# Performance work log

Hardware: AMD Instinct MI355X
Metric: run time of the kernel (lower is better)

The kernel has to match this reference:

```python
import math
import jax, jax.numpy as jnp
import numpy as np

H = 8
DIM = 256
HD = DIM // H
SCALE = math.sqrt(HD)
EPS = 1e-16


def _segment_softmax(scores, dst, num_nodes):
    # scores: [E, H], dst: [E] -> softmax over edges sharing the same dst
    m = jax.ops.segment_max(scores, dst, num_segments=num_nodes)  # [N, H]
    m = jnp.where(jnp.isfinite(m), m, 0.0)  # empty segments -> -inf -> 0
    e = jnp.exp(scores - m[dst])
    s = jax.ops.segment_sum(e, dst, num_segments=num_nodes)  # [N, H]
    return e / (s[dst] + EPS)


def _graph_attention(x, edges, wq, bq, wk, bk, wv, bv, wo, bo):
    # x: [N, DIM]; edges: [2, E] (src, dst). Dropout is identity (eval mode).
    N = x.shape[0]
    Q = (x @ wq + bq).reshape(N, H, HD)
    K = (x @ wk + bk).reshape(N, H, HD)
    V = (x @ wv + bv).reshape(N, H, HD)
    src, dst = edges[0], edges[1]
    scores = jnp.einsum('ehd,ehd->eh', Q[dst], K[src]) / SCALE  # [E, H]
    attn = _segment_softmax(scores, dst, N)  # [E, H]
    msgs = V[src] * attn[:, :, None]  # [E, H, HD]
    out = jax.ops.segment_sum(msgs, dst, num_segments=N).reshape(N, DIM)
    return out @ wo + bo


def _linear_params(key, fan_in, fan_out):
    k1, k2 = jax.random.split(key)
    bound = 1.0 / math.sqrt(fan_in)
    w = jax.random.uniform(k1, (fan_in, fan_out), minval=-bound, maxval=bound, dtype=jnp.float32)
    b = jax.random.uniform(k2, (fan_out,), minval=-bound, maxval=bound, dtype=jnp.float32)
    return w, b


def setup_inputs() -> dict:
    key = jax.random.key(0)
    ks = jax.random.split(key, 12)
    n_slot, n_dom = 20000, 1000
    e_slot, e_dom = 320000, 16000
    inp = {
        'slot_x': jax.random.normal(ks[0], (n_slot, DIM), dtype=jnp.float32),
        'domain_x': jax.random.normal(ks[1], (n_dom, DIM), dtype=jnp.float32),
        'slot_edges': jax.random.randint(ks[2], (2, e_slot), 0, n_slot, dtype=jnp.int32),
        'domain_edges': jax.random.randint(ks[3], (2, e_dom), 0, n_dom, dtype=jnp.int32),
    }
    names = ['wq', 'wk', 'wv', 'wo']
    for i, nm in enumerate(names):
        w, b = _linear_params(ks[4 + i], DIM, DIM)
        inp[f'slot_{nm}'] = w
        inp[f'slot_{nm}_b'] = b
    for i, nm in enumerate(names):
        w, b = _linear_params(ks[8 + i], DIM, DIM)
        inp[f'dom_{nm}'] = w
        inp[f'dom_{nm}_b'] = b
    return inp


def reference(slot_x, domain_x, slot_edges, domain_edges,
              slot_wq, slot_wq_b, slot_wk, slot_wk_b, slot_wv, slot_wv_b, slot_wo, slot_wo_b,
              dom_wq, dom_wq_b, dom_wk, dom_wk_b, dom_wv, dom_wv_b, dom_wo, dom_wo_b):
    # slot branch: self-attention on slot graph + identity residual
    slot_out = _graph_attention(slot_x, slot_edges,
                                slot_wq, slot_wq_b, slot_wk, slot_wk_b,
                                slot_wv, slot_wv_b, slot_wo, slot_wo_b) + slot_x
    # domain branch
    dom_out = _graph_attention(domain_x, domain_edges,
                               dom_wq, dom_wq_b, dom_wk, dom_wk_b,
                               dom_wv, dom_wv_b, dom_wo, dom_wo_b) + domain_x
    return slot_out, dom_out
```

## Files before the change

kernel.cpp:

```cpp
#include <hip/hip_runtime.h>
#include <hip/hip_bf16.h>

#define DIM 256
#define INV_SCALE 0.17677669529663687f
#define SM_EPS 1e-16f
#define BM 128
#define BN 64
#define BK 32

typedef unsigned short ushortT;
typedef unsigned int uintT;
typedef __attribute__((ext_vector_type(8))) __bf16 bf16x8;
typedef __attribute__((ext_vector_type(4))) float f32x4;

__device__ __forceinline__ float bf2f(ushortT u) {
    return __uint_as_float(((uintT)u) << 16);
}
__device__ __forceinline__ ushortT f2bf(float f) {
    uintT u = __float_as_uint(f);
    u += 0x7FFFu + ((u >> 16) & 1u);
    return (ushortT)(u >> 16);
}

struct WPack { const void* w[8]; const void* b[8]; };

__device__ __forceinline__ bool sniff_m16(const ushortT* __restrict__ x) {
    int lane = threadIdx.x & 63;
    ushortT u = x[lane * 2];
    int e = (u >> 7) & 0xFF;
    bool sane = ((u & 0x7FFFu) == 0) || (e >= 0x66 && e <= 0x90);
    unsigned long long m = __ballot(sane);
    return __popcll(m) >= 32;
}

__global__ __launch_bounds__(256) void megaA(
        const void* __restrict__ xs, const void* __restrict__ xd,
        const ushortT* __restrict__ sniff_src,
        ushortT* __restrict__ xb_s, ushortT* __restrict__ xb_d,
        WPack pk, ushortT* __restrict__ wT, float* __restrict__ biasF,
        int* __restrict__ cnt_s, int* __restrict__ cnt_d,
        uintT* __restrict__ st_s, uintT* __restrict__ st_d,
        int* __restrict__ done, int* __restrict__ flagWs,
        int n4s, int n4d, int Ns_, int Nd_, int nbN_, int nbD_,
        int nA0, int nA1, int nA2)
{
    const bool m16 = sniff_m16(sniff_src);
    const int bid = blockIdx.x;
    const int t = threadIdx.x;

    if (bid < nA0 + nA1) {
        const bool d = bid >= nA0;
        const int li = d ? bid - nA0 : bid;
        const int n4 = d ? n4d : n4s;
        const int i = li * 256 + t;
        if (i >= n4) return;
        const void* x = d ? xd : xs;
        ushortT* xb = d ? xb_d : xb_s;
        if (m16) {
            ((ushort4*)xb)[i] = ((const ushort4*)x)[i];
        } else {
            float4 v = ((const float4*)x)[i];
            ushort4 o2;
            o2.x = f2bf(v.x); o2.y = f2bf(v.y); o2.z = f2bf(v.z); o2.w = f2bf(v.w);
            ((ushort4*)xb)[i] = o2;
        }
    } else if (bid < nA0 + nA1 + nA2) {
        const int r = bid - (nA0 + nA1);
        const int which = r / 257;
        const int j = r % 257;
        if (j == 256) {
            const void* b = pk.b[which];
            float v = m16 ? bf2f(((const ushortT*)b)[t]) : ((const float*)b)[t];
            biasF[which * 256 + t] = v;
        } else {
            const void* w = pk.w[which];
            float v = m16 ? bf2f(((const ushortT*)w)[t * 256 + j])
                          : ((const float*)w)[t * 256 + j];
            wT[(size_t)which * 65536 + j * 256 + t] = f2bf(v);
        }
    } else {
        const int li = bid - (nA0 + nA1 + nA2);
        const int idx = li * 256 + t;
        if (idx < Ns_) { cnt_s[idx] = 0; return; }
        int k = idx - Ns_;
        if (k < Nd_) { cnt_d[k] = 0; return; }
        k -= Nd_;
        if (k < nbN_) { st_s[k] = 0; return; }
        k -= nbN_;
        if (k < nbD_) { st_d[k] = 0; return; }
        k -= nbD_;
        if (k == 0) *done = 0;
        else if (k == 1) *flagWs = m16 ? 1 : 0;
    }
}

__device__ __forceinline__ void gemm_core(const ushortT* __restrict__ A,
                                          const ushortT* __restrict__ BT,
                                          int row0, int col0, int M,
                                          f32x4 (&acc)[2][4]) {
    __shared__ ushortT As[BM * BK];
    __shared__ ushortT Bs[BN * BK];
    const int tid  = threadIdx.x;
    const int wid  = tid >> 6;
    const int lane = tid & 63;
    const int r_i = tid >> 2;
    const int kq8 = (tid & 3) << 3;
    const int m   = lane & 15;
    const int q   = lane >> 4;

    const size_t rA0 = (size_t)min(row0 + r_i, M - 1) * DIM;
    const size_t rA1 = (size_t)min(row0 + 64 + r_i, M - 1) * DIM;
    const size_t rB  = (size_t)(col0 + r_i) * DIM;

    for (int k0 = 0; k0 < DIM; k0 += BK) {
        uint4 a0v = *(const uint4*)(A + rA0 + k0 + kq8);
        uint4 a1v = *(const uint4*)(A + rA1 + k0 + kq8);
        uint4 bv  = *(const uint4*)(BT + rB + k0 + kq8);
        __syncthreads();
        *(uint4*)&As[r_i * BK + kq8]        = a0v;
        *(uint4*)&As[(64 + r_i) * BK + kq8] = a1v;
        *(uint4*)&Bs[r_i * BK + kq8]        = bv;
        __syncthreads();

        bf16x8 af0 = *(const bf16x8*)&As[(wid * 32 + m) * BK + q * 8];
        bf16x8 af1 = *(const bf16x8*)&As[(wid * 32 + 16 + m) * BK + q * 8];
        #pragma unroll
        for (int j = 0; j < 4; ++j) {
            bf16x8 bf = *(const bf16x8*)&Bs[(j * 16 + m) * BK + q * 8];
            acc[0][j] = __builtin_amdgcn_mfma_f32_16x16x32_bf16(af0, bf, acc[0][j], 0, 0, 0);
            acc[1][j] = __builtin_amdgcn_mfma_f32_16x16x32_bf16(af1, bf, acc[1][j], 0, 0, 0);
        }
    }
}

__global__ __launch_bounds__(256) void megaB(
        const ushortT* __restrict__ xb_s, const ushortT* __restrict__ xb_d,
        const ushortT* __restrict__ wT, const float* __restrict__ biasF,
        ushortT* __restrict__ qkv_s, ushortT* __restrict__ qkv_d,
        size_t zss, size_t zsd, int Ms, int Md, int nbs_, int nbq_,
        const int* __restrict__ dst_s, const int* __restrict__ dst_d,
        int* __restrict__ cnt_s, int* __restrict__ cnt_d, int Es_, int Ed_)
{
    const int bid = blockIdx.x;
    const int nq = nbq_ * 12;
    if (bid >= nq) {
        const int idx = (bid - nq) * 256 + threadIdx.x;
        if (idx < Es_) atomicAdd(&cnt_s[dst_s[idx]], 1);
        else { int e = idx - Es_; if (e < Ed_) atomicAdd(&cnt_d[dst_d[e]], 1); }
        return;
    }
    const int z  = bid / (nbq_ * 4);
    const int r  = bid % (nbq_ * 4);
    const int by = r / nbq_;
    const int bx0 = r % nbq_;
    const bool dom = bx0 >= nbs_;
    const int bx = dom ? bx0 - nbs_ : bx0;
    const ushortT* A = dom ? xb_d : xb_s;
    const int M = dom ? Md : Ms;
    const int widx = z + (dom ? 4 : 0);
    const ushortT* BT = wT + (size_t)widx * 65536;
    const float* bias = biasF + widx * 256;
    ushortT* C = (dom ? qkv_d : qkv_s) + (size_t)z * (dom ? zsd : zss);

    const int row0 = bx * BM;
    const int col0 = by * BN;
    const int wid = threadIdx.x >> 6, lane = threadIdx.x & 63;
    const int m = lane & 15, q = lane >> 4;

    f32x4 acc[2][4];
    #pragma unroll
    for (int i = 0; i < 2; ++i)
        #pragma unroll
        for (int j = 0; j < 4; ++j) acc[i][j] = (f32x4){0.f, 0.f, 0.f, 0.f};

    gemm_core(A, BT, row0, col0, M, acc);

    #pragma unroll
    for (int i = 0; i < 2; ++i)
        #pragma unroll
        for (int j = 0; j < 4; ++j) {
            const int col = col0 + j * 16 + m;
            const float bval = bias[col];
            #pragma unroll
            for (int rr = 0; rr < 4; ++rr) {
                const int row = row0 + wid * 32 + i * 16 + q * 4 + rr;
                if (row < M)
                    C[(size_t)row * DIM + col] = f2bf(acc[i][j][rr] + bval);
            }
        }
}

__device__ __forceinline__ uintT spack(uintT st, uintT v) { return (st << 30) | v; }

__global__ __launch_bounds__(256) void scan_scatter(
        const int* __restrict__ cnt_s, const int* __restrict__ cnt_d,
        uintT* __restrict__ st_s, uintT* __restrict__ st_d,
        int* __restrict__ rp_s, int* __restrict__ rp_d,
        int* __restrict__ cur_s, int* __restrict__ cur_d,
        int* __restrict__ done,
        const int* __restrict__ ss, const int* __restrict__ ds,
        const int* __restrict__ sd, const int* __restrict__ dd,
        int* __restrict__ col_s, int* __restrict__ col_d,
        int Ns_, int Nd_, int nbN_, int nbD_, int Es_, int Ed_)
{
    __shared__ int sh[256];
    __shared__ int exclS;
    const int b = blockIdx.x;
    const int t = threadIdx.x;
    const bool dom = b >= nbN_;
    const int lb = dom ? b - nbN_ : b;
    const int N = dom ? Nd_ : Ns_;
    const int* cnt = dom ? cnt_d : cnt_s;
    uintT* st = dom ? st_d : st_s;
    int* rp = dom ? rp_d : rp_s;
    int* cur = dom ? cur_d : cur_s;

    const int i = lb * 256 + t;
    const int v = (i < N) ? cnt[i] : 0;
    sh[t] = v;
    __syncthreads();
    for (int off = 1; off < 256; off <<= 1) {
        int u = (t >= off) ? sh[t - off] : 0;
        __syncthreads();
        sh[t] += u;
        __syncthreads();
    }

    if (t == 0) {
        const uintT agg = (uintT)sh[255];
        uintT excl = 0;
        if (lb == 0) {
            __hip_atomic_store(&st[0], spack(2u, agg), __ATOMIC_RELEASE,
                               __HIP_MEMORY_SCOPE_AGENT);
        } else {
            __hip_atomic_store(&st[lb], spack(1u, agg), __ATOMIC_RELEASE,
                               __HIP_MEMORY_SCOPE_AGENT);
            int j = lb - 1;
            while (j >= 0) {
                uintT s = __hip_atomic_load(&st[j], __ATOMIC_ACQUIRE,
                                            __HIP_MEMORY_SCOPE_AGENT);
                uintT tag = s >> 30;
                if (tag == 2u) { excl += s & 0x3FFFFFFFu; break; }
                if (tag == 1u) { excl += s & 0x3FFFFFFFu; --j; }
            }
            __hip_atomic_store(&st[lb], spack(2u, excl + agg), __ATOMIC_RELEASE,
                               __HIP_MEMORY_SCOPE_AGENT);
        }
        exclS = (int)excl;
    }
    __syncthreads();
    const int excl = exclS;
    if (i < N) {
        const int e = excl + ((t == 0) ? 0 : sh[t - 1]);
        rp[i] = e;
        cur[i] = e;
        if (i == N - 1) rp[N] = e + v;
    }

    __threadfence();
    __syncthreads();
    if (t == 0) {
        __hip_atomic_fetch_add(done, 1, __ATOMIC_ACQ_REL, __HIP_MEMORY_SCOPE_AGENT);
        const int nb = nbN_ + nbD_;
        while (__hip_atomic_load(done, __ATOMIC_ACQUIRE, __HIP_MEMORY_SCOPE_AGENT) < nb) {}
    }
    __syncthreads();

    const int total = Es_ + Ed_;
    const int stride = (nbN_ + nbD_) * 256;
    for (int idx = b * 256 + t; idx < total; idx += stride) {
        if (idx < Es_) {
            int pos = atomicAdd(&cur_s[ds[idx]], 1);
            col_s[pos] = ss[idx];
        } else {
            int e = idx - Es_;
            int pos = atomicAdd(&cur_d[dd[e]], 1);
            col_d[pos] = sd[e];
        }
    }
}

__global__ __launch_bounds__(256) void attn_kernel(
        const ushortT* __restrict__ Qs, const ushortT* __restrict__ Ks,
        const ushortT* __restrict__ Vs, const int* __restrict__ rps,
        const int* __restrict__ css, ushortT* __restrict__ aggs,
        const ushortT* __restrict__ Qd_, const ushortT* __restrict__ Kd_,
        const ushortT* __restrict__ Vd_, const int* __restrict__ rpd,
        const int* __restrict__ csd, ushortT* __restrict__ aggd,
        int Ns_, int Ntot)
{
    const int sub = threadIdx.x & 31;
    const int g = blockIdx.x * 8 + (threadIdx.x >> 5);
    if (g >= Ntot) return;
    const bool dom = g >= Ns_;
    const int d = dom ? g - Ns_ : g;
    const ushortT* Qb = dom ? Qd_ : Qs;
    const ushortT* Kb = dom ? Kd_ : Ks;
    const ushortT* Vb = dom ? Vd_ : Vs;
    const int* rowptr = dom ? rpd : rps;
    const int* colsrc = dom ? csd : css;
    ushortT* aggb = dom ? aggd : aggs;

    const int c8 = sub * 8;
    const size_t cbase = (size_t)d * DIM + c8;

    uint4 qv = *(const uint4*)(Qb + cbase);
    float qf[8];
    qf[0] = bf2f((ushortT)(qv.x & 0xFFFF)); qf[1] = bf2f((ushortT)(qv.x >> 16));
    qf[2] = bf2f((ushortT)(qv.y & 0xFFFF)); qf[3] = bf2f((ushortT)(qv.y >> 16));
    qf[4] = bf2f((ushortT)(qv.z & 0xFFFF)); qf[5] = bf2f((ushortT)(qv.z >> 16));
    qf[6] = bf2f((ushortT)(qv.w & 0xFFFF)); qf[7] = bf2f((ushortT)(qv.w >> 16));

    float acc[8] = {};
    float den = 0.f;

    auto PROC = [&](uint4 kv, uint4 vv) {
        float kf[8];
        kf[0] = bf2f((ushortT)(kv.x & 0xFFFF)); kf[1] = bf2f((ushortT)(kv.x >> 16));
        kf[2] = bf2f((ushortT)(kv.y & 0xFFFF)); kf[3] = bf2f((ushortT)(kv.y >> 16));
        kf[4] = bf2f((ushortT)(kv.z & 0xFFFF)); kf[5] = bf2f((ushortT)(kv.z >> 16));
        kf[6] = bf2f((ushortT)(kv.w & 0xFFFF)); kf[7] = bf2f((ushortT)(kv.w >> 16));
        float p = qf[0] * kf[0] + qf[1] * kf[1] + qf[2] * kf[2] + qf[3] * kf[3]
                + qf[4] * kf[4] + qf[5] * kf[5] + qf[6] * kf[6] + qf[7] * kf[7];
        p += __shfl_xor(p, 1, 4);
        p += __shfl_xor(p, 2, 4);
        const float w = __expf(fminf(p * INV_SCALE, 60.0f));
        den += w;
        acc[0] += w * bf2f((ushortT)(vv.x & 0xFFFF));
        acc[1] += w * bf2f((ushortT)(vv.x >> 16));
        acc[2] += w * bf2f((ushortT)(vv.y & 0xFFFF));
        acc[3] += w * bf2f((ushortT)(vv.y >> 16));
        acc[4] += w * bf2f((ushortT)(vv.z & 0xFFFF));
        acc[5] += w * bf2f((ushortT)(vv.z >> 16));
        acc[6] += w * bf2f((ushortT)(vv.w & 0xFFFF));
        acc[7] += w * bf2f((ushortT)(vv.w >> 16));
    };

    const int beg = rowptr[d], end = rowptr[d + 1];
    int i = beg;
    for (; i + 4 <= end; i += 4) {
        const int s0 = colsrc[i], s1 = colsrc[i + 1];
        const int s2 = colsrc[i + 2], s3 = colsrc[i + 3];
        const size_t b0 = (size_t)s0 * DIM + c8, b1 = (size_t)s1 * DIM + c8;
        const size_t b2 = (size_t)s2 * DIM + c8, b3 = (size_t)s3 * DIM + c8;
        uint4 k0v = *(const uint4*)(Kb + b0), v0v = *(const uint4*)(Vb + b0);
        uint4 k1v = *(const uint4*)(Kb + b1), v1v = *(const uint4*)(Vb + b1);
        uint4 k2v = *(const uint4*)(Kb + b2), v2v = *(const uint4*)(Vb + b2);
        uint4 k3v = *(const uint4*)(Kb + b3), v3v = *(const uint4*)(Vb + b3);
        PROC(k0v, v0v); PROC(k1v, v1v); PROC(k2v, v2v); PROC(k3v, v3v);
    }
    for (; i < end; ++i) {
        const size_t sb = (size_t)colsrc[i] * DIM + c8;
        PROC(*(const uint4*)(Kb + sb), *(const uint4*)(Vb + sb));
    }

    const float r = 1.0f / (den + SM_EPS);
    uint4 o;
    o.x = (uintT)f2bf(acc[0] * r) | ((uintT)f2bf(acc[1] * r) << 16);
    o.y = (uintT)f2bf(acc[2] * r) | ((uintT)f2bf(acc[3] * r) << 16);
    o.z = (uintT)f2bf(acc[4] * r) | ((uintT)f2bf(acc[5] * r) << 16);
    o.w = (uintT)f2bf(acc[6] * r) | ((uintT)f2bf(acc[7] * r) << 16);
    *(uint4*)(aggb + cbase) = o;
}

__global__ __launch_bounds__(256) void gemm_out(
        const ushortT* __restrict__ As_, const ushortT* __restrict__ Ad_,
        const ushortT* __restrict__ wT, const float* __restrict__ biasF,
        const void* __restrict__ xs, const void* __restrict__ xd,
        void* __restrict__ dout, int Ms, int Md, int nbs,
        const int* __restrict__ flag)
{
    const bool dom = (int)blockIdx.x >= nbs;
    const int bx = dom ? blockIdx.x - nbs : blockIdx.x;
    const ushortT* A = dom ? Ad_ : As_;
    const int M = dom ? Md : Ms;
    const int widx = 3 + (dom ? 4 : 0);
    const ushortT* BT = wT + (size_t)widx * 65536;
    const float* bias = biasF + widx * 256;
    const void* res = dom ? xd : xs;
    const size_t outOff = dom ? (size_t)Ms * DIM : 0;

    const int row0 = bx * BM;
    const int col0 = blockIdx.y * BN;
    const int wid = threadIdx.x >> 6, lane = threadIdx.x & 63;
    const int m = lane & 15, q = lane >> 4;

    f32x4 acc[2][4];
    #pragma unroll
    for (int i = 0; i < 2; ++i)
        #pragma unroll
        for (int j = 0; j < 4; ++j) acc[i][j] = (f32x4){0.f, 0.f, 0.f, 0.f};

    gemm_core(A, BT, row0, col0, M, acc);

    const bool m16 = (*flag != 0);
    #pragma unroll
    for (int i = 0; i < 2; ++i)
        #pragma unroll
        for (int j = 0; j < 4; ++j) {
            const int col = col0 + j * 16 + m;
            const float bval = bias[col];
            #pragma unroll
            for (int r = 0; r < 4; ++r) {
                const int row = row0 + wid * 32 + i * 16 + q * 4 + r;
                if (row < M) {
                    const size_t ridx = (size_t)row * DIM + col;
                    float v = acc[i][j][r] + bval;
                    v += m16 ? bf2f(((const ushortT*)res)[ridx])
                             : ((const float*)res)[ridx];
                    if (m16) ((ushortT*)dout)[outOff + ridx] = f2bf(v);
                    else     ((float*)dout)[outOff + ridx] = v;
                }
            }
        }
}

extern "C" void kernel_launch(void* const* d_in, const int* in_sizes, int n_in,
                              void* d_out, int out_size, void* d_ws, size_t ws_size,
                              hipStream_t stream)
{
    const void* slot_x = d_in[0];
    const void* dom_x  = d_in[1];
    const int* slot_edges = (const int*)d_in[2];
    const int* dom_edges  = (const int*)d_in[3];
    const int Ns = in_sizes[0] / DIM;
    const int Nd = in_sizes[1] / DIM;
    const int Es = in_sizes[2] / 2;
    const int Ed = in_sizes[3] / 2;

    WPack pk;
    for (int i = 0; i < 8; ++i) { pk.w[i] = d_in[4 + 2 * i]; pk.b[i] = d_in[5 + 2 * i]; }

    char* p = (char*)d_ws;
    size_t o = 0;
    auto take = [&](size_t b) { void* r = p + o; o = (o + b + 255) & ~(size_t)255; return r; };
    const size_t ndS = (size_t)Ns * DIM;
    const size_t ndD = (size_t)Nd * DIM;
    ushortT* xb_s  = (ushortT*)take(ndS * 2);
    ushortT* qkv_s = (ushortT*)take(3 * ndS * 2);
    ushortT* agg_s = (ushortT*)take(ndS * 2);
    ushortT* xb_d  = (ushortT*)take(ndD * 2);
    ushortT* qkv_d = (ushortT*)take(3 * ndD * 2);
    ushortT* agg_d = (ushortT*)take(ndD * 2);
    ushortT* wT    = (ushortT*)take(8 * 65536 * 2);
    float*   biasF = (float*)take(8 * 256 * 4);
    int* rp_s  = (int*)take((size_t)(Ns + 1) * 4);
    int* cur_s = (int*)take((size_t)Ns * 4);
    int* cnt_s = (int*)take((size_t)Ns * 4);
    int* col_s = (int*)take((size_t)Es * 4);
    int* rp_d  = (int*)take((size_t)(Nd + 1) * 4);
    int* cur_d = (int*)take((size_t)Nd * 4);
    int* cnt_d = (int*)take((size_t)Nd * 4);
    int* col_d = (int*)take((size_t)Ed * 4);
    uintT* st_s = (uintT*)take(512 * 4);
    uintT* st_d = (uintT*)take(256 * 4);
    int* done   = (int*)take(256);
    int* flagWs = (int*)take(256);

    const int* src_s = slot_edges;
    const int* dst_s = slot_edges + Es;
    const int* src_d = dom_edges;
    const int* dst_d = dom_edges + Ed;

    const int n4s = Ns * DIM / 4, n4d = Nd * DIM / 4;
    const int nbN = (Ns + 255) / 256;
    const int nbD = (Nd + 255) / 256;
    const int nbs = (Ns + BM - 1) / BM;
    const int nbd = (Nd + BM - 1) / BM;
    const int nbq = nbs + nbd;

    const int nA0 = (n4s + 255) / 256;
    const int nA1 = (n4d + 255) / 256;
    const int nA2 = 257 * 8;
    const int nZ  = (Ns + Nd + nbN + nbD + 2 + 255) / 256;
    hipLaunchKernelGGL(megaA, dim3(nA0 + nA1 + nA2 + nZ), dim3(256), 0, stream,
                       slot_x, dom_x, (const ushortT*)slot_x, xb_s, xb_d,
                       pk, wT, biasF, cnt_s, cnt_d, st_s, st_d, done, flagWs,
                       n4s, n4d, Ns, Nd, nbN, nbD, nA0, nA1, nA2);

    const int nCnt = (Es + Ed + 255) / 256;
    hipLaunchKernelGGL(megaB, dim3(nbq * 12 + nCnt), dim3(256), 0, stream,
                       xb_s, xb_d, wT, biasF, qkv_s, qkv_d, ndS, ndD,
                       Ns, Nd, nbs, nbq, dst_s, dst_d, cnt_s, cnt_d, Es, Ed);

    hipLaunchKernelGGL(scan_scatter, dim3(nbN + nbD), dim3(256), 0, stream,
                       cnt_s, cnt_d, st_s, st_d, rp_s, rp_d, cur_s, cur_d, done,
                       src_s, dst_s, src_d, dst_d, col_s, col_d,
                       Ns, Nd, nbN, nbD, Es, Ed);

    const int Ntot = Ns + Nd;
    hipLaunchKernelGGL(attn_kernel, dim3((Ntot + 7) / 8), dim3(256), 0, stream,
                       qkv_s, qkv_s + ndS, qkv_s + 2 * ndS, rp_s, col_s, agg_s,
                       qkv_d, qkv_d + ndD, qkv_d + 2 * ndD, rp_d, col_d, agg_d,
                       Ns, Ntot);

    hipLaunchKernelGGL(gemm_out, dim3(nbq, DIM / BN), dim3(256), 0, stream,
                       agg_s, agg_d, wT, biasF, slot_x, dom_x, d_out,
                       Ns, Nd, nbs, flagWs);
}
```

Baseline: 271.5 us.

## Split scan/scatter kernel at grid barrier and deepen attention gather unroll

The combined scan_scatter kernel used a spin-wait grid barrier on a global counter before scattering edges with only ~83 blocks. It is now split into scan_nodes and a separate scatter_edges kernel with one thread per edge, so the kernel boundary replaces the barrier and the scatter runs across many more blocks. The attention gather loop also gains an 8-edge unrolled stage that issues all K/V loads before processing them, to keep more memory requests in flight. The costs are one extra kernel launch and higher register pressure in the attention kernel.

```diff
diff --git a/kernel.cpp b/kernel.cpp
--- a/kernel.cpp
+++ b/kernel.cpp
@@ -192,16 +192,12 @@
 
 __device__ __forceinline__ uintT spack(uintT st, uintT v) { return (st << 30) | v; }
 
-__global__ __launch_bounds__(256) void scan_scatter(
+__global__ __launch_bounds__(256) void scan_nodes(
         const int* __restrict__ cnt_s, const int* __restrict__ cnt_d,
         uintT* __restrict__ st_s, uintT* __restrict__ st_d,
         int* __restrict__ rp_s, int* __restrict__ rp_d,
         int* __restrict__ cur_s, int* __restrict__ cur_d,
-        int* __restrict__ done,
-        const int* __restrict__ ss, const int* __restrict__ ds,
-        const int* __restrict__ sd, const int* __restrict__ dd,
-        int* __restrict__ col_s, int* __restrict__ col_d,
-        int Ns_, int Nd_, int nbN_, int nbD_, int Es_, int Ed_)
+        int Ns_, int Nd_, int nbN_)
 {
     __shared__ int sh[256];
     __shared__ int exclS;
@@ -256,24 +252,22 @@
         cur[i] = e;
         if (i == N - 1) rp[N] = e + v;
     }
-
-    __threadfence();
-    __syncthreads();
-    if (t == 0) {
-        __hip_atomic_fetch_add(done, 1, __ATOMIC_ACQ_REL, __HIP_MEMORY_SCOPE_AGENT);
-        const int nb = nbN_ + nbD_;
-        while (__hip_atomic_load(done, __ATOMIC_ACQUIRE, __HIP_MEMORY_SCOPE_AGENT) < nb) {}
-    }
-    __syncthreads();
-
-    const int total = Es_ + Ed_;
-    const int stride = (nbN_ + nbD_) * 256;
-    for (int idx = b * 256 + t; idx < total; idx += stride) {
-        if (idx < Es_) {
-            int pos = atomicAdd(&cur_s[ds[idx]], 1);
-            col_s[pos] = ss[idx];
-        } else {
-            int e = idx - Es_;
+}
+
+__global__ __launch_bounds__(256) void scatter_edges(
+        const int* __restrict__ ss, const int* __restrict__ ds,
+        const int* __restrict__ sd, const int* __restrict__ dd,
+        int* __restrict__ cur_s, int* __restrict__ cur_d,
+        int* __restrict__ col_s, int* __restrict__ col_d,
+        int Es_, int Ed_)
+{
+    const int idx = blockIdx.x * 256 + threadIdx.x;
+    if (idx < Es_) {
+        int pos = atomicAdd(&cur_s[ds[idx]], 1);
+        col_s[pos] = ss[idx];
+    } else {
+        int e = idx - Es_;
+        if (e < Ed_) {
             int pos = atomicAdd(&cur_d[dd[e]], 1);
             col_d[pos] = sd[e];
         }
@@ -338,16 +332,27 @@
 
     const int beg = rowptr[d], end = rowptr[d + 1];
     int i = beg;
+    for (; i + 8 <= end; i += 8) {
+        uint4 kv[8], vv[8];
+        #pragma unroll
+        for (int j = 0; j < 8; ++j) {
+            const size_t b = (size_t)colsrc[i + j] * DIM + c8;
+            kv[j] = *(const uint4*)(Kb + b);
+            vv[j] = *(const uint4*)(Vb + b);
+        }
+        #pragma unroll
+        for (int j = 0; j < 8; ++j) PROC(kv[j], vv[j]);
+    }
     for (; i + 4 <= end; i += 4) {
-        const int s0 = colsrc[i], s1 = colsrc[i + 1];
-        const int s2 = colsrc[i + 2], s3 = colsrc[i + 3];
-        const size_t b0 = (size_t)s0 * DIM + c8, b1 = (size_t)s1 * DIM + c8;
-        const size_t b2 = (size_t)s2 * DIM + c8, b3 = (size_t)s3 * DIM + c8;
-        uint4 k0v = *(const uint4*)(Kb + b0), v0v = *(const uint4*)(Vb + b0);
-        uint4 k1v = *(const uint4*)(Kb + b1), v1v = *(const uint4*)(Vb + b1);
-        uint4 k2v = *(const uint4*)(Kb + b2), v2v = *(const uint4*)(Vb + b2);
-        uint4 k3v = *(const uint4*)(Kb + b3), v3v = *(const uint4*)(Vb + b3);
-        PROC(k0v, v0v); PROC(k1v, v1v); PROC(k2v, v2v); PROC(k3v, v3v);
+        uint4 kv[4], vv[4];
+        #pragma unroll
+        for (int j = 0; j < 4; ++j) {
+            const size_t b = (size_t)colsrc[i + j] * DIM + c8;
+            kv[j] = *(const uint4*)(Kb + b);
+            vv[j] = *(const uint4*)(Vb + b);
+        }
+        #pragma unroll
+        for (int j = 0; j < 4; ++j) PROC(kv[j], vv[j]);
     }
     for (; i < end; ++i) {
         const size_t sb = (size_t)colsrc[i] * DIM + c8;
@@ -483,10 +488,12 @@
                        xb_s, xb_d, wT, biasF, qkv_s, qkv_d, ndS, ndD,
                        Ns, Nd, nbs, nbq, dst_s, dst_d, cnt_s, cnt_d, Es, Ed);
 
-    hipLaunchKernelGGL(scan_scatter, dim3(nbN + nbD), dim3(256), 0, stream,
-                       cnt_s, cnt_d, st_s, st_d, rp_s, rp_d, cur_s, cur_d, done,
-                       src_s, dst_s, src_d, dst_d, col_s, col_d,
-                       Ns, Nd, nbN, nbD, Es, Ed);
+    hipLaunchKernelGGL(scan_nodes, dim3(nbN + nbD), dim3(256), 0, stream,
+                       cnt_s, cnt_d, st_s, st_d, rp_s, rp_d, cur_s, cur_d,
+                       Ns, Nd, nbN);
+    hipLaunchKernelGGL(scatter_edges, dim3(nCnt), dim3(256), 0, stream,
+                       src_s, dst_s, src_d, dst_d, cur_s, cur_d, col_s, col_d,
+                       Es, Ed);
 
     const int Ntot = Ns + Nd;
     hipLaunchKernelGGL(attn_kernel, dim3((Ntot + 7) / 8), dim3(256), 0, stream,
```

Measured after the change: 274.5 us. No clear change (+1.1%).
